# Kernel optimization log

Hardware: AMD Instinct MI355X
Metric: run time of the kernel (lower is better)

Reference implementation:

```python
import jax, jax.numpy as jnp
import numpy as np

N = 2048       # agent nodes
D = 128        # latent_dim
H = 64         # hidden width of edge MLP


def setup_inputs() -> dict:
    key = jax.random.key(0)
    k_z, k_w1, k_w2, k_eps = jax.random.split(key, 4)
    z = jax.random.normal(k_z, (N + 1, D), dtype=jnp.float32)
    # nn.Linear(3D, 64) weight stored as (in, out) for right-multiplication
    W1 = jax.random.normal(k_w1, (3 * D, H), dtype=jnp.float32) / np.sqrt(3 * D)
    b1 = jnp.zeros((H,), dtype=jnp.float32)
    W2 = jax.random.normal(k_w2, (H, 1), dtype=jnp.float32) / np.sqrt(H)
    b2 = jnp.zeros((1,), dtype=jnp.float32)
    # uniform noise standing in for torch.rand_like(w) in the training branch
    eps = jax.random.uniform(k_eps, (N, N), dtype=jnp.float32)
    return {"z": z, "W1": W1, "b1": b1, "W2": W2, "b2": b2, "eps": eps}


def reference(z, W1, b1, W2, b2, eps):
    # z: (N+1, D); last row is the task node
    agent = z[:-1]                      # (N, D)
    task = z[-1]                        # (D,)
    # Decompose Linear(3D->H) over the concat [h_i, h_j, task]:
    # combined @ W1 = h_i @ W1a + h_j @ W1b + task @ W1c
    W1a, W1b, W1c = W1[:D], W1[D:2 * D], W1[2 * D:]
    pi = agent @ W1a                    # (N, H) row term
    pj = agent @ W1b                    # (N, H) col term
    pt = task @ W1c + b1                # (H,)   shared task term + bias
    h = jax.nn.relu(pi[:, None, :] + pj[None, :, :] + pt)   # (N, N, H)
    w = jnp.einsum('ijh,h->ij', h, W2[:, 0]) + b2[0]         # (N, N) edge logits
    # Gumbel-sigmoid (training branch), temperature = 1.0
    e = eps + 1e-8
    gumbel = jnp.log(e) - jnp.log(1.0 - e)
    return jax.nn.sigmoid(w + gumbel)
```

## Files before the change

kernel.cpp:

```cpp
#include <hip/hip_runtime.h>

#define NN 2048
#define DD 128
#define HH 64

__global__ __launch_bounds__(256) void proj_kernel(
    const float* __restrict__ z, const float* __restrict__ W1,
    const float* __restrict__ b1, float* __restrict__ pi, float* __restrict__ pjt)
{
    __shared__ float sA[16][DD];
    __shared__ float sT[DD];
    const int t = threadIdx.x;
    const int rowBase = blockIdx.x * 16;

    #pragma unroll
    for (int c = 0; c < 2; ++c) {
        int idx = c * 256 + t;
        int rr  = idx >> 5;
        int kq  = idx & 31;
        float4 v = *(const float4*)(z + (rowBase + rr) * DD + kq * 4);
        *(float4*)(&sA[rr][kq * 4]) = v;
    }
    if (t < DD / 4) {
        float4 v = *(const float4*)(z + (size_t)NN * DD + t * 4);
        *(float4*)(&sT[t * 4]) = v;
    }
    __syncthreads();

    const int h  = t & 63;
    const int rg = t >> 6;

    float ai[4] = {0.f, 0.f, 0.f, 0.f};
    float aj[4] = {0.f, 0.f, 0.f, 0.f};
    float at = 0.f;
    #pragma unroll 4
    for (int k = 0; k < DD; ++k) {
        const float w1a = W1[k * HH + h];
        const float w1b = W1[(DD + k) * HH + h];
        const float w1c = W1[(2 * DD + k) * HH + h];
        at = fmaf(sT[k], w1c, at);
        #pragma unroll
        for (int a = 0; a < 4; ++a) {
            const float av = sA[rg * 4 + a][k];
            ai[a] = fmaf(av, w1a, ai[a]);
            aj[a] = fmaf(av, w1b, aj[a]);
        }
    }
    const float ptv = at + b1[h];
    #pragma unroll
    for (int a = 0; a < 4; ++a) {
        const int row = rowBase + rg * 4 + a;
        pi[row * HH + h]  = ai[a];
        pjt[row * HH + h] = aj[a] + ptv;
    }
}

__global__ __launch_bounds__(256, 2) void pair_kernel(
    const float* __restrict__ pi, const float* __restrict__ pjt,
    const float* __restrict__ W2, const float* __restrict__ b2,
    const float* __restrict__ eps, float* __restrict__ out)
{
    __shared__ float sPi[HH][132];
    __shared__ float sPj[HH][68];

    const int t  = threadIdx.x;
    const int i0 = blockIdx.y * 128;
    const int j0 = blockIdx.x * 64;

    #pragma unroll
    for (int c = 0; c < 2; ++c) {
        const int g  = c * 256 + t;
        const int hq = g & 15;
        const int ig = g >> 4;
        const float* src = pi + (size_t)(i0 + ig * 4) * HH + hq * 4;
        float4 v0 = *(const float4*)(src);
        float4 v1 = *(const float4*)(src + HH);
        float4 v2 = *(const float4*)(src + 2 * HH);
        float4 v3 = *(const float4*)(src + 3 * HH);
        *(float4*)(&sPi[hq * 4 + 0][ig * 4]) = make_float4(v0.x, v1.x, v2.x, v3.x);
        *(float4*)(&sPi[hq * 4 + 1][ig * 4]) = make_float4(v0.y, v1.y, v2.y, v3.y);
        *(float4*)(&sPi[hq * 4 + 2][ig * 4]) = make_float4(v0.z, v1.z, v2.z, v3.z);
        *(float4*)(&sPi[hq * 4 + 3][ig * 4]) = make_float4(v0.w, v1.w, v2.w, v3.w);
    }
    {
        const int hq = t & 15;
        const int jg = t >> 4;
        const float* src = pjt + (size_t)(j0 + jg * 4) * HH + hq * 4;
        float4 v0 = *(const float4*)(src);
        float4 v1 = *(const float4*)(src + HH);
        float4 v2 = *(const float4*)(src + 2 * HH);
        float4 v3 = *(const float4*)(src + 3 * HH);
        *(float4*)(&sPj[hq * 4 + 0][jg * 4]) = make_float4(v0.x, v1.x, v2.x, v3.x);
        *(float4*)(&sPj[hq * 4 + 1][jg * 4]) = make_float4(v0.y, v1.y, v2.y, v3.y);
        *(float4*)(&sPj[hq * 4 + 2][jg * 4]) = make_float4(v0.z, v1.z, v2.z, v3.z);
        *(float4*)(&sPj[hq * 4 + 3][jg * 4]) = make_float4(v0.w, v1.w, v2.w, v3.w);
    }

    const int lane = t & 63;
    const int wv   = t >> 6;
    const int ib   = (wv >> 1) * 64 + (lane >> 3) * 8;
    const int jb   = (wv & 1) * 32 + (lane & 7) * 4;

    float4 eps4[8];
    #pragma unroll
    for (int r = 0; r < 8; ++r)
        eps4[r] = *(const float4*)(eps + (size_t)(i0 + ib + r) * NN + (j0 + jb));

    __syncthreads();

    float acc[8][4];
    #pragma unroll
    for (int r = 0; r < 8; ++r)
        #pragma unroll
        for (int c = 0; c < 4; ++c) acc[r][c] = 0.f;

    #pragma unroll 4
    for (int h = 0; h < HH; ++h) {
        const float4 a0 = *(const float4*)(&sPi[h][ib]);
        const float4 a1 = *(const float4*)(&sPi[h][ib + 4]);
        const float4 bv = *(const float4*)(&sPj[h][jb]);
        const float w2h = W2[h];
        const float ai[8] = {a0.x, a0.y, a0.z, a0.w, a1.x, a1.y, a1.z, a1.w};
        const float bj[4] = {bv.x, bv.y, bv.z, bv.w};
        #pragma unroll
        for (int r = 0; r < 8; ++r)
            #pragma unroll
            for (int c = 0; c < 4; ++c)
                acc[r][c] = fmaf(fmaxf(ai[r] + bj[c], 0.f), w2h, acc[r][c]);
    }

    const float b2v = b2[0];
    #pragma unroll
    for (int r = 0; r < 8; ++r) {
        const size_t base = (size_t)(i0 + ib + r) * NN + (j0 + jb);
        const float4 e4 = eps4[r];
        float4 o;
        {
            float e = e4.x + 1e-8f, w = acc[r][0] + b2v;
            o.x = __fdividef(e, e + (1.f - e) * __expf(-w));
        }
        {
            float e = e4.y + 1e-8f, w = acc[r][1] + b2v;
            o.y = __fdividef(e, e + (1.f - e) * __expf(-w));
        }
        {
            float e = e4.z + 1e-8f, w = acc[r][2] + b2v;
            o.z = __fdividef(e, e + (1.f - e) * __expf(-w));
        }
        {
            float e = e4.w + 1e-8f, w = acc[r][3] + b2v;
            o.w = __fdividef(e, e + (1.f - e) * __expf(-w));
        }
        *(float4*)(out + base) = o;
    }
}

extern "C" void kernel_launch(void* const* d_in, const int* in_sizes, int n_in,
                              void* d_out, int out_size, void* d_ws, size_t ws_size,
                              hipStream_t stream) {
    const float* z   = (const float*)d_in[0];
    const float* W1  = (const float*)d_in[1];
    const float* b1  = (const float*)d_in[2];
    const float* W2  = (const float*)d_in[3];
    const float* b2  = (const float*)d_in[4];
    const float* eps = (const float*)d_in[5];
    float* out = (float*)d_out;

    float* pi  = (float*)d_ws;
    float* pjt = pi + (size_t)NN * HH;

    proj_kernel<<<NN / 16, 256, 0, stream>>>(z, W1, b1, pi, pjt);
    pair_kernel<<<dim3(NN / 64, NN / 128), 256, 0, stream>>>(pi, pjt, W2, b2, eps, out);
}
```

Baseline: 115.5 us.

## Use packed fp16 pair math with fdot2 in the edge MLP inner loop

Measured after the change: 110.0 us. 4.8% less time.

```diff
diff --git a/kernel.cpp b/kernel.cpp
--- a/kernel.cpp
+++ b/kernel.cpp
@@ -4,9 +4,23 @@
 #define DD 128
 #define HH 64
 
+typedef _Float16 half2v __attribute__((ext_vector_type(2)));
+
+static __device__ __forceinline__ unsigned pack_h2(float x, float y) {
+    half2v v;
+    v.x = (_Float16)x;
+    v.y = (_Float16)y;
+    return __builtin_bit_cast(unsigned, v);
+}
+static __device__ __forceinline__ half2v unpack_h2(unsigned u) {
+    return __builtin_bit_cast(half2v, u);
+}
+
 __global__ __launch_bounds__(256) void proj_kernel(
     const float* __restrict__ z, const float* __restrict__ W1,
-    const float* __restrict__ b1, float* __restrict__ pi, float* __restrict__ pjt)
+    const float* __restrict__ b1, const float* __restrict__ W2,
+    unsigned* __restrict__ piH, unsigned* __restrict__ pjtH,
+    unsigned* __restrict__ w2pair)
 {
     __shared__ float sA[16][DD];
     __shared__ float sT[DD];
@@ -25,75 +39,80 @@
         float4 v = *(const float4*)(z + (size_t)NN * DD + t * 4);
         *(float4*)(&sT[t * 4]) = v;
     }
+    if (blockIdx.x == 0 && t < HH / 2)
+        w2pair[t] = pack_h2(W2[2 * t], W2[2 * t + 1]);
     __syncthreads();
 
-    const int h  = t & 63;
-    const int rg = t >> 6;
-
-    float ai[4] = {0.f, 0.f, 0.f, 0.f};
-    float aj[4] = {0.f, 0.f, 0.f, 0.f};
-    float at = 0.f;
+    const int h2 = t & 31;
+    const int rg = t >> 5;
+
+    float ai[2][2] = {{0.f,0.f},{0.f,0.f}};
+    float aj[2][2] = {{0.f,0.f},{0.f,0.f}};
+    float at[2] = {0.f, 0.f};
     #pragma unroll 4
     for (int k = 0; k < DD; ++k) {
-        const float w1a = W1[k * HH + h];
-        const float w1b = W1[(DD + k) * HH + h];
-        const float w1c = W1[(2 * DD + k) * HH + h];
-        at = fmaf(sT[k], w1c, at);
+        const float2 wa = *(const float2*)(W1 + (size_t)k * HH + 2 * h2);
+        const float2 wb = *(const float2*)(W1 + (size_t)(DD + k) * HH + 2 * h2);
+        const float2 wc = *(const float2*)(W1 + (size_t)(2 * DD + k) * HH + 2 * h2);
+        const float tv = sT[k];
+        at[0] = fmaf(tv, wc.x, at[0]);
+        at[1] = fmaf(tv, wc.y, at[1]);
         #pragma unroll
-        for (int a = 0; a < 4; ++a) {
-            const float av = sA[rg * 4 + a][k];
-            ai[a] = fmaf(av, w1a, ai[a]);
-            aj[a] = fmaf(av, w1b, aj[a]);
-        }
-    }
-    const float ptv = at + b1[h];
-    #pragma unroll
-    for (int a = 0; a < 4; ++a) {
-        const int row = rowBase + rg * 4 + a;
-        pi[row * HH + h]  = ai[a];
-        pjt[row * HH + h] = aj[a] + ptv;
+        for (int r = 0; r < 2; ++r) {
+            const float av = sA[rg * 2 + r][k];
+            ai[r][0] = fmaf(av, wa.x, ai[r][0]);
+            ai[r][1] = fmaf(av, wa.y, ai[r][1]);
+            aj[r][0] = fmaf(av, wb.x, aj[r][0]);
+            aj[r][1] = fmaf(av, wb.y, aj[r][1]);
+        }
+    }
+    const float pt0 = at[0] + b1[2 * h2];
+    const float pt1 = at[1] + b1[2 * h2 + 1];
+    #pragma unroll
+    for (int r = 0; r < 2; ++r) {
+        const int row = rowBase + rg * 2 + r;
+        piH [row * (HH/2) + h2] = pack_h2(ai[r][0], ai[r][1]);
+        pjtH[row * (HH/2) + h2] = pack_h2(aj[r][0] + pt0, aj[r][1] + pt1);
     }
 }
 
 __global__ __launch_bounds__(256, 2) void pair_kernel(
-    const float* __restrict__ pi, const float* __restrict__ pjt,
-    const float* __restrict__ W2, const float* __restrict__ b2,
+    const unsigned* __restrict__ piH, const unsigned* __restrict__ pjtH,
+    const unsigned* __restrict__ w2pair, const float* __restrict__ b2,
     const float* __restrict__ eps, float* __restrict__ out)
 {
-    __shared__ float sPi[HH][132];
-    __shared__ float sPj[HH][68];
+    __shared__ unsigned sPi[HH/2][132];
+    __shared__ unsigned sPj[HH/2][68];
 
     const int t  = threadIdx.x;
     const int i0 = blockIdx.y * 128;
     const int j0 = blockIdx.x * 64;
 
-    #pragma unroll
-    for (int c = 0; c < 2; ++c) {
-        const int g  = c * 256 + t;
-        const int hq = g & 15;
-        const int ig = g >> 4;
-        const float* src = pi + (size_t)(i0 + ig * 4) * HH + hq * 4;
-        float4 v0 = *(const float4*)(src);
-        float4 v1 = *(const float4*)(src + HH);
-        float4 v2 = *(const float4*)(src + 2 * HH);
-        float4 v3 = *(const float4*)(src + 3 * HH);
-        *(float4*)(&sPi[hq * 4 + 0][ig * 4]) = make_float4(v0.x, v1.x, v2.x, v3.x);
-        *(float4*)(&sPi[hq * 4 + 1][ig * 4]) = make_float4(v0.y, v1.y, v2.y, v3.y);
-        *(float4*)(&sPi[hq * 4 + 2][ig * 4]) = make_float4(v0.z, v1.z, v2.z, v3.z);
-        *(float4*)(&sPi[hq * 4 + 3][ig * 4]) = make_float4(v0.w, v1.w, v2.w, v3.w);
-    }
     {
-        const int hq = t & 15;
-        const int jg = t >> 4;
-        const float* src = pjt + (size_t)(j0 + jg * 4) * HH + hq * 4;
-        float4 v0 = *(const float4*)(src);
-        float4 v1 = *(const float4*)(src + HH);
-        float4 v2 = *(const float4*)(src + 2 * HH);
-        float4 v3 = *(const float4*)(src + 3 * HH);
-        *(float4*)(&sPj[hq * 4 + 0][jg * 4]) = make_float4(v0.x, v1.x, v2.x, v3.x);
-        *(float4*)(&sPj[hq * 4 + 1][jg * 4]) = make_float4(v0.y, v1.y, v2.y, v3.y);
-        *(float4*)(&sPj[hq * 4 + 2][jg * 4]) = make_float4(v0.z, v1.z, v2.z, v3.z);
-        *(float4*)(&sPj[hq * 4 + 3][jg * 4]) = make_float4(v0.w, v1.w, v2.w, v3.w);
+        const int ig = t & 31;
+        const int hq = t >> 5;
+        const unsigned* src = piH + (size_t)(i0 + ig * 4) * (HH/2) + hq * 4;
+        uint4 v0 = *(const uint4*)(src);
+        uint4 v1 = *(const uint4*)(src + (HH/2));
+        uint4 v2 = *(const uint4*)(src + 2 * (HH/2));
+        uint4 v3 = *(const uint4*)(src + 3 * (HH/2));
+        *(uint4*)(&sPi[hq * 4 + 0][ig * 4]) = make_uint4(v0.x, v1.x, v2.x, v3.x);
+        *(uint4*)(&sPi[hq * 4 + 1][ig * 4]) = make_uint4(v0.y, v1.y, v2.y, v3.y);
+        *(uint4*)(&sPi[hq * 4 + 2][ig * 4]) = make_uint4(v0.z, v1.z, v2.z, v3.z);
+        *(uint4*)(&sPi[hq * 4 + 3][ig * 4]) = make_uint4(v0.w, v1.w, v2.w, v3.w);
+    }
+    if (t < 128) {
+        const int jg = t & 15;
+        const int hq = t >> 4;
+        const unsigned* src = pjtH + (size_t)(j0 + jg * 4) * (HH/2) + hq * 4;
+        uint4 v0 = *(const uint4*)(src);
+        uint4 v1 = *(const uint4*)(src + (HH/2));
+        uint4 v2 = *(const uint4*)(src + 2 * (HH/2));
+        uint4 v3 = *(const uint4*)(src + 3 * (HH/2));
+        *(uint4*)(&sPj[hq * 4 + 0][jg * 4]) = make_uint4(v0.x, v1.x, v2.x, v3.x);
+        *(uint4*)(&sPj[hq * 4 + 1][jg * 4]) = make_uint4(v0.y, v1.y, v2.y, v3.y);
+        *(uint4*)(&sPj[hq * 4 + 2][jg * 4]) = make_uint4(v0.z, v1.z, v2.z, v3.z);
+        *(uint4*)(&sPj[hq * 4 + 3][jg * 4]) = make_uint4(v0.w, v1.w, v2.w, v3.w);
     }
 
     const int lane = t & 63;
@@ -114,19 +133,32 @@
         #pragma unroll
         for (int c = 0; c < 4; ++c) acc[r][c] = 0.f;
 
+    const half2v hz = (half2v)(_Float16)0;
+
     #pragma unroll 4
-    for (int h = 0; h < HH; ++h) {
-        const float4 a0 = *(const float4*)(&sPi[h][ib]);
-        const float4 a1 = *(const float4*)(&sPi[h][ib + 4]);
-        const float4 bv = *(const float4*)(&sPj[h][jb]);
-        const float w2h = W2[h];
-        const float ai[8] = {a0.x, a0.y, a0.z, a0.w, a1.x, a1.y, a1.z, a1.w};
-        const float bj[4] = {bv.x, bv.y, bv.z, bv.w};
+    for (int h2 = 0; h2 < HH / 2; ++h2) {
+        const uint4 A0 = *(const uint4*)(&sPi[h2][ib]);
+        const uint4 A1 = *(const uint4*)(&sPi[h2][ib + 4]);
+        const uint4 B  = *(const uint4*)(&sPj[h2][jb]);
+        const unsigned w2u = w2pair[h2];
+        const half2v w2h = unpack_h2(w2u);
+        const unsigned au[8] = {A0.x, A0.y, A0.z, A0.w, A1.x, A1.y, A1.z, A1.w};
+        const unsigned bu[4] = {B.x, B.y, B.z, B.w};
         #pragma unroll
-        for (int r = 0; r < 8; ++r)
+        for (int r = 0; r < 8; ++r) {
+            const half2v ah = unpack_h2(au[r]);
             #pragma unroll
-            for (int c = 0; c < 4; ++c)
-                acc[r][c] = fmaf(fmaxf(ai[r] + bj[c], 0.f), w2h, acc[r][c]);
+            for (int c = 0; c < 4; ++c) {
+                half2v s = ah + unpack_h2(bu[c]);
+                s = __builtin_elementwise_max(s, hz);
+#if __has_builtin(__builtin_amdgcn_fdot2)
+                acc[r][c] = __builtin_amdgcn_fdot2(s, w2h, acc[r][c], false);
+#else
+                acc[r][c] = fmaf((float)s.x, (float)w2h.x,
+                            fmaf((float)s.y, (float)w2h.y, acc[r][c]));
+#endif
+            }
+        }
     }
 
     const float b2v = b2[0];
@@ -166,9 +198,10 @@
     const float* eps = (const float*)d_in[5];
     float* out = (float*)d_out;
 
-    float* pi  = (float*)d_ws;
-    float* pjt = pi + (size_t)NN * HH;
-
-    proj_kernel<<<NN / 16, 256, 0, stream>>>(z, W1, b1, pi, pjt);
-    pair_kernel<<<dim3(NN / 64, NN / 128), 256, 0, stream>>>(pi, pjt, W2, b2, eps, out);
-}
+    unsigned* piH    = (unsigned*)d_ws;
+    unsigned* pjtH   = piH + (size_t)NN * (HH / 2);
+    unsigned* w2pair = pjtH + (size_t)NN * (HH / 2);
+
+    proj_kernel<<<NN / 16, 256, 0, stream>>>(z, W1, b1, W2, piH, pjtH, w2pair);
+    pair_kernel<<<dim3(NN / 64, NN / 128), 256, 0, stream>>>(piH, pjtH, w2pair, b2, eps, out);
+}
```
